# Performance work log

Measured on AMD Instinct MI355X. Metric: run time of the kernel, lower is better.

## Reference

```python
import jax, jax.numpy as jnp
import numpy as np

MASK_FILL = -99999.0  # value used by masked_fill_ in the torch source


def setup_inputs() -> dict:
    key = jax.random.key(0)
    k1, k2, k3, k4, k5, k6, k7 = jax.random.split(key, 7)
    B, S, H = 8, 2048, 1024
    query = jax.random.normal(k1, (B, S, H), dtype=jnp.float32)
    key_t = jax.random.normal(k2, (B, S, H), dtype=jnp.float32)
    value = jax.random.normal(k3, (B, S, H), dtype=jnp.float32)
    mask = jax.random.randint(k4, (B, S), 0, 2, dtype=jnp.int32)
    s = 1.0 / np.sqrt(H)
    Wq = jax.random.uniform(k5, (H, H), dtype=jnp.float32, minval=-s, maxval=s)
    Wk = jax.random.uniform(k6, (H, H), dtype=jnp.float32, minval=-s, maxval=s)
    Wv = jax.random.uniform(k7, (H, H), dtype=jnp.float32, minval=-s, maxval=s)
    return {"query": query, "key": key_t, "value": value,
            "Wq": Wq, "Wk": Wk, "Wv": Wv, "mask": mask}


def reference(query, key, value, Wq, Wk, Wv, mask):
    # Linear(h,h,bias=False): y = x @ W.T
    q = jnp.einsum('bsh,oh->bso', query, Wq)
    k = jnp.einsum('bsh,oh->bso', key, Wk)
    v = jnp.einsum('bsh,oh->bso', value, Wv)
    # score[b,i,j] = q[b,i,:] . k[b,j,:]  (NO 1/sqrt(d) scaling in source)
    score = jnp.einsum('bqh,bkh->bqk', q, k)
    # mask: [B, S_k] -> [B, 1, S_k]; positions where mask==0 get MASK_FILL
    m = mask[:, None, :]
    score = jnp.where(m == 0, jnp.float32(MASK_FILL), score)
    attn = jax.nn.softmax(score, axis=-1)
    context = jnp.einsum('bqk,bkh->bqh', attn, v)
    return context
```

## Files before the change

### kernel.cpp

```cpp
#include <hip/hip_runtime.h>
#include <hip/hip_fp16.h>
#include <math.h>

typedef _Float16 f16;
typedef _Float16 f16x4 __attribute__((ext_vector_type(4)));
typedef _Float16 f16x8 __attribute__((ext_vector_type(8)));
typedef float f32x4 __attribute__((ext_vector_type(4)));

#define GLOAD_LDS16(g, l)                                                                  \
    __builtin_amdgcn_global_load_lds((const __attribute__((address_space(1))) void*)(g),   \
                                     (__attribute__((address_space(3))) void*)(l), 16, 0, 0)

__global__ __launch_bounds__(256) void cast3_kernel(const float* __restrict__ s0,
                                                    const float* __restrict__ s1,
                                                    const float* __restrict__ s2,
                                                    f16* d0, f16* d1, f16* d2, int n16each)
{
    const int z = blockIdx.z;
    const float* src = (z == 0) ? s0 : (z == 1) ? s1 : s2;
    f16* dst = (z == 0) ? d0 : (z == 1) ? d1 : d2;
    const int stride = gridDim.x * blockDim.x;
    for (int i = blockIdx.x * blockDim.x + threadIdx.x; i < n16each; i += stride) {
        const float4* sp = (const float4*)(src + (long long)i * 16);
        float4 a = sp[0], b = sp[1], c = sp[2], d4 = sp[3];
        f16x8 lo = {(f16)a.x, (f16)a.y, (f16)a.z, (f16)a.w,
                    (f16)b.x, (f16)b.y, (f16)b.z, (f16)b.w};
        f16x8 hi = {(f16)c.x, (f16)c.y, (f16)c.z, (f16)c.w,
                    (f16)d4.x, (f16)d4.y, (f16)d4.z, (f16)d4.w};
        f16x8* dp = (f16x8*)(dst + (long long)i * 16);
        dp[0] = lo;
        dp[1] = hi;
    }
}

template <int OUTF16, int TRANSC>
__global__ __launch_bounds__(512, 2) void gemm_nt_k(
    const f16* __restrict__ Ab, const f16* __restrict__ Bb, void* __restrict__ Cb,
    int K, int lda, int ldb, int ldc,
    long long sA, long long sB, long long sC, int gx)
{
    __shared__ __align__(16) f16 smem[256 * 64 + 128 * 64];

    const int nwg = gridDim.x;
    const int swz = (blockIdx.x & 7) * (nwg >> 3) + (blockIdx.x >> 3);
    const int bx = swz % gx, by = swz / gx;

    const int z = blockIdx.z;
    const char* pA = (const char*)(Ab + z * sA + (long long)by * 256 * lda);
    const char* pB = (const char*)(Bb + z * sB + (long long)bx * 128 * ldb);
    const long long lda2 = (long long)lda * 2, ldb2 = (long long)ldb * 2;

    const int tid = threadIdx.x;
    const int w = tid >> 6, l = tid & 63;
    const int wr = w >> 1, wc = w & 1;

    f32x4 acc[4][4];
#pragma unroll
    for (int i = 0; i < 4; i++)
#pragma unroll
        for (int j = 0; j < 4; j++) acc[i][j] = (f32x4){0.f, 0.f, 0.f, 0.f};

    const int lr = l & 15;
    const int lkb = (l >> 4) * 16;

#define FRAG_A(row, kbyte)                                                                \
    (*(const f16x8*)((const char*)&smem[0] + ((row) * 128) + ((kbyte) ^ (((row) & 7) << 4))))
#define FRAG_B(row, kbyte)                                                                \
    (*(const f16x8*)((const char*)&smem[0] + 32768 + ((row) * 128) + ((kbyte) ^ (((row) & 7) << 4))))

    const int nt = K >> 6;
    for (int t = 0; t < nt; ++t) {
        const long long kb = (long long)t * 128;
#pragma unroll
        for (int i = 0; i < 4; i++) {
            const int c = i * 512 + tid;
            const int row = c >> 3;
            const int col = ((c & 7) * 16) ^ ((row & 7) << 4);
            GLOAD_LDS16(pA + (long long)row * lda2 + kb + col, &smem[(long long)c * 8]);
        }
#pragma unroll
        for (int i = 0; i < 2; i++) {
            const int c = i * 512 + tid;
            const int row = c >> 3;
            const int col = ((c & 7) * 16) ^ ((row & 7) << 4);
            GLOAD_LDS16(pB + (long long)row * ldb2 + kb + col, &smem[16384 + (long long)c * 8]);
        }
        __syncthreads();

        f16x8 bf[4][2], af[4][2];
#pragma unroll
        for (int fc = 0; fc < 4; fc++)
#pragma unroll
            for (int ks = 0; ks < 2; ks++)
                bf[fc][ks] = FRAG_B(wc * 64 + fc * 16 + lr, ks * 64 + lkb);
#pragma unroll
        for (int fq = 0; fq < 4; fq++)
#pragma unroll
            for (int ks = 0; ks < 2; ks++)
                af[fq][ks] = FRAG_A(wr * 64 + fq * 16 + lr, ks * 64 + lkb);

#pragma unroll
        for (int fq = 0; fq < 4; fq++)
#pragma unroll
            for (int fc = 0; fc < 4; fc++)
#pragma unroll
                for (int ks = 0; ks < 2; ks++)
                    acc[fq][fc] = __builtin_amdgcn_mfma_f32_16x16x32_f16(
                        af[fq][ks], bf[fc][ks], acc[fq][fc], 0, 0, 0);

        __syncthreads();
    }
#undef FRAG_A
#undef FRAG_B

    const int row_l = (l >> 4) * 4;
    const long long gr0 = (long long)by * 256 + wr * 64;
    const int gc0 = bx * 128 + wc * 64;

    if (TRANSC) {
        const long long blk_r0 = (long long)by * 256;
        const int b = (int)(blk_r0 >> 11);
        const int s_base = (int)(blk_r0 & 2047);
        f16* vTp = (f16*)Cb + (long long)b * 1024 * 2048;
#pragma unroll
        for (int h = 0; h < 2; h++) {
            __syncthreads();
            if ((wr >> 1) == h) {
                const int s64 = (wr & 1) * 64;
#pragma unroll
                for (int fq = 0; fq < 4; fq++)
#pragma unroll
                    for (int fc = 0; fc < 4; fc++)
#pragma unroll
                        for (int i = 0; i < 4; i++)
                            smem[(wc * 64 + fc * 16 + lr) * 136 + s64 + fq * 16 + row_l + i] =
                                (f16)acc[fq][fc][i];
            }
            __syncthreads();
#pragma unroll
            for (int j = 0; j < 4; j++) {
                const int c = j * 512 + tid;
                const int o = c >> 4, s8 = (c & 15) * 8;
                f16x8 vv = *(const f16x8*)&smem[o * 136 + s8];
                *(f16x8*)&vTp[((long long)(bx * 128 + o)) * 2048 + s_base + h * 128 + s8] = vv;
            }
        }
    } else if (OUTF16) {
        f16* C = (f16*)Cb + z * sC;
#pragma unroll
        for (int fq = 0; fq < 4; fq++)
#pragma unroll
            for (int fc = 0; fc < 4; fc++)
#pragma unroll
                for (int i = 0; i < 4; i++)
                    C[(gr0 + fq * 16 + row_l + i) * ldc + gc0 + fc * 16 + lr] = (f16)acc[fq][fc][i];
    } else {
        float* C = (float*)Cb + z * sC;
#pragma unroll
        for (int fq = 0; fq < 4; fq++)
#pragma unroll
            for (int fc = 0; fc < 4; fc++)
#pragma unroll
                for (int i = 0; i < 4; i++)
                    C[(gr0 + fq * 16 + row_l + i) * ldc + gc0 + fc * 16 + lr] = acc[fq][fc][i];
    }
}

__device__ __forceinline__ float wred_max(float v) {
#pragma unroll
    for (int o = 32; o > 0; o >>= 1) v = fmaxf(v, __shfl_xor(v, o));
    return v;
}
__device__ __forceinline__ float wred_sum(float v) {
#pragma unroll
    for (int o = 32; o > 0; o >>= 1) v += __shfl_xor(v, o);
    return v;
}

__global__ __launch_bounds__(256) void softmax_kernel(f16* __restrict__ Sm, const int* __restrict__ mask)
{
    const long long row = blockIdx.x;
    const int b = (int)(row >> 11);
    f16* Srow = Sm + row * 2048;
    const int* mrow = mask + b * 2048;
    const int t = threadIdx.x;
    const int w = t >> 6, l = t & 63;

    f16x8 sv = *(const f16x8*)(Srow + t * 8);
    int4 m0 = *(const int4*)(mrow + t * 8);
    int4 m1 = *(const int4*)(mrow + t * 8 + 4);
    int mk[8] = {m0.x, m0.y, m0.z, m0.w, m1.x, m1.y, m1.z, m1.w};
    float v[8];
#pragma unroll
    for (int j = 0; j < 8; j++) v[j] = (float)sv[j];

    float mx = -INFINITY;
#pragma unroll
    for (int j = 0; j < 8; j++) if (mk[j]) mx = fmaxf(mx, v[j]);
    mx = wred_max(mx);
    __shared__ float redm[4], reds[4];
    if (l == 0) redm[w] = mx;
    __syncthreads();
    mx = fmaxf(fmaxf(redm[0], redm[1]), fmaxf(redm[2], redm[3]));

    if (mx == -INFINITY) {
        const f16 u = (f16)(1.0f / 2048.0f);
        f16x8 pv;
#pragma unroll
        for (int j = 0; j < 8; j++) pv[j] = u;
        *(f16x8*)(Srow + t * 8) = pv;
        return;
    }

    float e[8];
    float s = 0.f;
#pragma unroll
    for (int j = 0; j < 8; j++) { e[j] = mk[j] ? expf(v[j] - mx) : 0.f; s += e[j]; }
    s = wred_sum(s);
    if (l == 0) reds[w] = s;
    __syncthreads();
    s = reds[0] + reds[1] + reds[2] + reds[3];
    const float inv = 1.0f / s;
    f16x8 pv;
#pragma unroll
    for (int j = 0; j < 8; j++) pv[j] = (f16)(e[j] * inv);
    *(f16x8*)(Srow + t * 8) = pv;
}

extern "C" void kernel_launch(void* const* d_in, const int* in_sizes, int n_in,
                              void* d_out, int out_size, void* d_ws, size_t ws_size,
                              hipStream_t stream)
{
    const float* query = (const float*)d_in[0];
    const float* keyi  = (const float*)d_in[1];
    const float* value = (const float*)d_in[2];
    const float* Wq    = (const float*)d_in[3];
    const float* Wk    = (const float*)d_in[4];
    const float* Wv    = (const float*)d_in[5];
    const int*   mask  = (const int*)d_in[6];
    float* out = (float*)d_out;

    const long long SH = (long long)8 * 2048 * 1024;
    f16* slot0 = (f16*)d_ws;
    f16* slot1 = slot0 + SH;
    f16* slot2 = slot0 + 2 * SH;
    f16* slot3 = slot0 + 3 * SH;
    f16* slot4 = slot0 + 4 * SH;
    f16* wh    = slot1;
    f16* Pb    = slot0;

    const int n16x = (int)(SH / 16);
    const int n16w = 1024 * 1024 / 16;
    const long long zero = 0;
    const long long M1 = 1024 * 1024;

    cast3_kernel<<<dim3(64, 1, 3), 256, 0, stream>>>(Wq, Wk, Wv, wh, wh + M1, wh + 2 * M1, n16w);
    cast3_kernel<<<dim3(1024, 1, 3), 256, 0, stream>>>(query, keyi, value, slot3, slot0, slot2, n16x);
    gemm_nt_k<1, 1><<<dim3(512, 1, 1), 512, 0, stream>>>(
        slot2, wh + 2 * M1, (void*)slot4, 1024, 1024, 1024, 2048, zero, zero, zero, 8);
    gemm_nt_k<1, 0><<<dim3(512, 1, 1), 512, 0, stream>>>(
        slot3, wh, (void*)slot2, 1024, 1024, 1024, 1024, zero, zero, zero, 8);
    gemm_nt_k<1, 0><<<dim3(512, 1, 1), 512, 0, stream>>>(
        slot0, wh + M1, (void*)slot3, 1024, 1024, 1024, 1024, zero, zero, zero, 8);
    gemm_nt_k<1, 0><<<dim3(128, 1, 8), 512, 0, stream>>>(
        slot2, slot3, (void*)Pb, 1024, 1024, 1024, 2048,
        (long long)2048 * 1024, (long long)2048 * 1024, (long long)2048 * 2048, 16);
    softmax_kernel<<<dim3(16384), 256, 0, stream>>>(Pb, mask);
    gemm_nt_k<0, 0><<<dim3(64, 1, 8), 512, 0, stream>>>(
        Pb, slot4, (void*)out, 2048, 2048, 2048, 1024,
        (long long)2048 * 2048, (long long)1024 * 2048, (long long)2048 * 1024, 8);
}
```

Before: 325.2 us.

## Fuse fp32-to-fp16 activation cast into projection GEMM A-tile loads

Removes the separate cast pass over query/key/value. The projection GEMMs now load fp32 A tiles straight into LDS with a wider swizzle and convert to fp16 when building fragments. This saves writing and re-reading three fp16 activation copies. In exchange it doubles the A tile's LDS footprint to 64KB plus 16KB for B, which may lower occupancy below two blocks per CU, and it adds conversion ALU work in the inner loop.

Measured after the change: 623.0 us. 91.6% more time.

```diff
diff --git a/kernel.cpp b/kernel.cpp
--- a/kernel.cpp
+++ b/kernel.cpp
@@ -33,22 +33,25 @@
     }
 }
 
-template <int OUTF16, int TRANSC>
+template <int OUTF16, int TRANSC, int AF32>
 __global__ __launch_bounds__(512, 2) void gemm_nt_k(
-    const f16* __restrict__ Ab, const f16* __restrict__ Bb, void* __restrict__ Cb,
+    const void* __restrict__ Ab, const f16* __restrict__ Bb, void* __restrict__ Cb,
     int K, int lda, int ldb, int ldc,
     long long sA, long long sB, long long sC, int gx)
 {
-    __shared__ __align__(16) f16 smem[256 * 64 + 128 * 64];
+    __shared__ __align__(16) f16 smem[AF32 ? (256 * 128 + 128 * 64) : (256 * 64 + 128 * 64)];
+    constexpr int B_OFF_E = AF32 ? 256 * 128 : 256 * 64;
+    constexpr int B_OFF_B = B_OFF_E * 2;
 
     const int nwg = gridDim.x;
     const int swz = (blockIdx.x & 7) * (nwg >> 3) + (blockIdx.x >> 3);
     const int bx = swz % gx, by = swz / gx;
 
     const int z = blockIdx.z;
-    const char* pA = (const char*)(Ab + z * sA + (long long)by * 256 * lda);
+    constexpr int esz = AF32 ? 4 : 2;
+    const char* pA = (const char*)Ab + ((long long)z * sA + (long long)by * 256 * lda) * esz;
     const char* pB = (const char*)(Bb + z * sB + (long long)bx * 128 * ldb);
-    const long long lda2 = (long long)lda * 2, ldb2 = (long long)ldb * 2;
+    const long long ldaB = (long long)lda * esz, ldb2 = (long long)ldb * 2;
 
     const int tid = threadIdx.x;
     const int w = tid >> 6, l = tid & 63;
@@ -63,27 +66,40 @@
     const int lr = l & 15;
     const int lkb = (l >> 4) * 16;
 
-#define FRAG_A(row, kbyte)                                                                \
+#define FRAG_A16(row, kbyte)                                                              \
     (*(const f16x8*)((const char*)&smem[0] + ((row) * 128) + ((kbyte) ^ (((row) & 7) << 4))))
 #define FRAG_B(row, kbyte)                                                                \
-    (*(const f16x8*)((const char*)&smem[0] + 32768 + ((row) * 128) + ((kbyte) ^ (((row) & 7) << 4))))
+    (*(const f16x8*)((const char*)&smem[0] + B_OFF_B + ((row) * 128) + ((kbyte) ^ (((row) & 7) << 4))))
 
     const int nt = K >> 6;
     for (int t = 0; t < nt; ++t) {
-        const long long kb = (long long)t * 128;
-#pragma unroll
-        for (int i = 0; i < 4; i++) {
-            const int c = i * 512 + tid;
-            const int row = c >> 3;
-            const int col = ((c & 7) * 16) ^ ((row & 7) << 4);
-            GLOAD_LDS16(pA + (long long)row * lda2 + kb + col, &smem[(long long)c * 8]);
+        const long long kb = (long long)t * 64 * esz;
+        if (AF32) {
+#pragma unroll
+            for (int i = 0; i < 8; i++) {
+                const int c = i * 512 + tid;
+                const int row = c >> 4;
+                const int col = ((c & 15) * 16) ^ ((row & 7) << 5);
+                GLOAD_LDS16(pA + (long long)row * ldaB + kb + col, &smem[(long long)c * 8]);
+            }
+        } else {
+#pragma unroll
+            for (int i = 0; i < 4; i++) {
+                const int c = i * 512 + tid;
+                const int row = c >> 3;
+                const int col = ((c & 7) * 16) ^ ((row & 7) << 4);
+                GLOAD_LDS16(pA + (long long)row * ldaB + kb + col, &smem[(long long)c * 8]);
+            }
         }
-#pragma unroll
-        for (int i = 0; i < 2; i++) {
-            const int c = i * 512 + tid;
-            const int row = c >> 3;
-            const int col = ((c & 7) * 16) ^ ((row & 7) << 4);
-            GLOAD_LDS16(pB + (long long)row * ldb2 + kb + col, &smem[16384 + (long long)c * 8]);
+        {
+            const long long kbB = (long long)t * 128;
+#pragma unroll
+            for (int i = 0; i < 2; i++) {
+                const int c = i * 512 + tid;
+                const int row = c >> 3;
+                const int col = ((c & 7) * 16) ^ ((row & 7) << 4);
+                GLOAD_LDS16(pB + (long long)row * ldb2 + kbB + col, &smem[B_OFF_E + (long long)c * 8]);
+            }
         }
         __syncthreads();
 
@@ -96,8 +112,19 @@
 #pragma unroll
         for (int fq = 0; fq < 4; fq++)
 #pragma unroll
-            for (int ks = 0; ks < 2; ks++)
-                af[fq][ks] = FRAG_A(wr * 64 + fq * 16 + lr, ks * 64 + lkb);
+            for (int ks = 0; ks < 2; ks++) {
+                const int row = wr * 64 + fq * 16 + lr;
+                if (AF32) {
+                    const int g0 = 2 * (ks * 64 + lkb);
+                    const char* base = (const char*)&smem[0] + row * 256 + ((g0) ^ ((row & 7) << 5));
+                    float4 lo = *(const float4*)(base);
+                    float4 hi = *(const float4*)(base + 16);
+                    af[fq][ks] = (f16x8){(f16)lo.x, (f16)lo.y, (f16)lo.z, (f16)lo.w,
+                                         (f16)hi.x, (f16)hi.y, (f16)hi.z, (f16)hi.w};
+                } else {
+                    af[fq][ks] = FRAG_A16(row, ks * 64 + lkb);
+                }
+            }
 
 #pragma unroll
         for (int fq = 0; fq < 4; fq++)
@@ -110,7 +137,7 @@
 
         __syncthreads();
     }
-#undef FRAG_A
+#undef FRAG_A16
 #undef FRAG_B
 
     const int row_l = (l >> 4) * 4;
@@ -249,24 +276,22 @@
     f16* wh    = slot1;
     f16* Pb    = slot0;
 
-    const int n16x = (int)(SH / 16);
     const int n16w = 1024 * 1024 / 16;
     const long long zero = 0;
     const long long M1 = 1024 * 1024;
 
     cast3_kernel<<<dim3(64, 1, 3), 256, 0, stream>>>(Wq, Wk, Wv, wh, wh + M1, wh + 2 * M1, n16w);
-    cast3_kernel<<<dim3(1024, 1, 3), 256, 0, stream>>>(query, keyi, value, slot3, slot0, slot2, n16x);
-    gemm_nt_k<1, 1><<<dim3(512, 1, 1), 512, 0, stream>>>(
-        slot2, wh + 2 * M1, (void*)slot4, 1024, 1024, 1024, 2048, zero, zero, zero, 8);
-    gemm_nt_k<1, 0><<<dim3(512, 1, 1), 512, 0, stream>>>(
-        slot3, wh, (void*)slot2, 1024, 1024, 1024, 1024, zero, zero, zero, 8);
-    gemm_nt_k<1, 0><<<dim3(512, 1, 1), 512, 0, stream>>>(
-        slot0, wh + M1, (void*)slot3, 1024, 1024, 1024, 1024, zero, zero, zero, 8);
-    gemm_nt_k<1, 0><<<dim3(128, 1, 8), 512, 0, stream>>>(
-        slot2, slot3, (void*)Pb, 1024, 1024, 1024, 2048,
+    gemm_nt_k<1, 1, 1><<<dim3(512, 1, 1), 512, 0, stream>>>(
+        (const void*)value, wh + 2 * M1, (void*)slot4, 1024, 1024, 1024, 2048, zero, zero, zero, 8);
+    gemm_nt_k<1, 0, 1><<<dim3(512, 1, 1), 512, 0, stream>>>(
+        (const void*)query, wh, (void*)slot2, 1024, 1024, 1024, 1024, zero, zero, zero, 8);
+    gemm_nt_k<1, 0, 1><<<dim3(512, 1, 1), 512, 0, stream>>>(
+        (const void*)keyi, wh + M1, (void*)slot3, 1024, 1024, 1024, 1024, zero, zero, zero, 8);
+    gemm_nt_k<1, 0, 0><<<dim3(128, 1, 8), 512, 0, stream>>>(
+        (const void*)slot2, slot3, (void*)Pb, 1024, 1024, 1024, 2048,
         (long long)2048 * 1024, (long long)2048 * 1024, (long long)2048 * 2048, 16);
     softmax_kernel<<<dim3(16384), 256, 0, stream>>>(Pb, mask);
-    gemm_nt_k<0, 0><<<dim3(64, 1, 8), 512, 0, stream>>>(
-        Pb, slot4, (void*)out, 2048, 2048, 2048, 1024,
+    gemm_nt_k<0, 0, 0><<<dim3(64, 1, 8), 512, 0, stream>>>(
+        (const void*)Pb, slot4, (void*)out, 2048, 2048, 2048, 1024,
         (long long)2048 * 2048, (long long)1024 * 2048, (long long)2048 * 1024, 8);
 }
```

## Fold Wq and Wk into one product matrix to skip a projection GEMM

Applied to the files above, without the earlier changes.

Precomputes M = Wq^T Wk (as a 1024x1024 fp16 matrix) using a transpose-cast kernel and a small GEMM. The score matrix is then formed as query · (key M^T)^T, so only the key is projected and the raw fp16 query is used directly, removing one of the large 16384x1024x1024 projection GEMMs. In exchange it adds a small weight GEMM and a transpose pass, and the fp16 rounding of the combined matrix changes numerical error. Scores here have large magnitude with no scaling, which can make this more sensitive.

Result: no change. 323.9 us (-0.4%).

```diff
diff --git a/kernel.cpp b/kernel.cpp
--- a/kernel.cpp
+++ b/kernel.cpp
@@ -33,6 +33,35 @@
     }
 }
 
+__global__ __launch_bounds__(256) void transcast_w_kernel(const float* __restrict__ Wq,
+                                                          const float* __restrict__ Wk,
+                                                          f16* __restrict__ dA,
+                                                          f16* __restrict__ dB)
+{
+    __shared__ f16 tile[64][72];
+    const float* src = blockIdx.z ? Wk : Wq;
+    f16* dst = blockIdx.z ? dB : dA;
+    const int h0 = blockIdx.x * 64, o0 = blockIdx.y * 64;
+    const int t = threadIdx.x;
+    const int r = t >> 2, c = (t & 3) * 16;
+    const float* sp = src + (long long)(o0 + r) * 1024 + h0 + c;
+    float4 v0 = *(const float4*)(sp + 0);
+    float4 v1 = *(const float4*)(sp + 4);
+    float4 v2 = *(const float4*)(sp + 8);
+    float4 v3 = *(const float4*)(sp + 12);
+    *(f16x4*)&tile[r][c]      = (f16x4){(f16)v0.x, (f16)v0.y, (f16)v0.z, (f16)v0.w};
+    *(f16x4*)&tile[r][c + 4]  = (f16x4){(f16)v1.x, (f16)v1.y, (f16)v1.z, (f16)v1.w};
+    *(f16x4*)&tile[r][c + 8]  = (f16x4){(f16)v2.x, (f16)v2.y, (f16)v2.z, (f16)v2.w};
+    *(f16x4*)&tile[r][c + 12] = (f16x4){(f16)v3.x, (f16)v3.y, (f16)v3.z, (f16)v3.w};
+    __syncthreads();
+    f16 buf[16];
+#pragma unroll
+    for (int j = 0; j < 16; j++) buf[j] = tile[c + j][r];
+    f16* dp = dst + (long long)(h0 + r) * 1024 + o0 + c;
+    *(f16x8*)(dp)     = *(f16x8*)&buf[0];
+    *(f16x8*)(dp + 8) = *(f16x8*)&buf[8];
+}
+
 template <int OUTF16, int TRANSC>
 __global__ __launch_bounds__(512, 2) void gemm_nt_k(
     const f16* __restrict__ Ab, const f16* __restrict__ Bb, void* __restrict__ Cb,
@@ -40,6 +69,8 @@
     long long sA, long long sB, long long sC, int gx)
 {
     __shared__ __align__(16) f16 smem[256 * 64 + 128 * 64];
+    constexpr int B_OFF_E = 256 * 64;
+    constexpr int B_OFF_B = B_OFF_E * 2;
 
     const int nwg = gridDim.x;
     const int swz = (blockIdx.x & 7) * (nwg >> 3) + (blockIdx.x >> 3);
@@ -63,10 +94,10 @@
     const int lr = l & 15;
     const int lkb = (l >> 4) * 16;
 
-#define FRAG_A(row, kbyte)                                                                \
+#define FRAG_A16(row, kbyte)                                                              \
     (*(const f16x8*)((const char*)&smem[0] + ((row) * 128) + ((kbyte) ^ (((row) & 7) << 4))))
 #define FRAG_B(row, kbyte)                                                                \
-    (*(const f16x8*)((const char*)&smem[0] + 32768 + ((row) * 128) + ((kbyte) ^ (((row) & 7) << 4))))
+    (*(const f16x8*)((const char*)&smem[0] + B_OFF_B + ((row) * 128) + ((kbyte) ^ (((row) & 7) << 4))))
 
     const int nt = K >> 6;
     for (int t = 0; t < nt; ++t) {
@@ -83,7 +114,7 @@
             const int c = i * 512 + tid;
             const int row = c >> 3;
             const int col = ((c & 7) * 16) ^ ((row & 7) << 4);
-            GLOAD_LDS16(pB + (long long)row * ldb2 + kb + col, &smem[16384 + (long long)c * 8]);
+            GLOAD_LDS16(pB + (long long)row * ldb2 + kb + col, &smem[B_OFF_E + (long long)c * 8]);
         }
         __syncthreads();
 
@@ -97,7 +128,7 @@
         for (int fq = 0; fq < 4; fq++)
 #pragma unroll
             for (int ks = 0; ks < 2; ks++)
-                af[fq][ks] = FRAG_A(wr * 64 + fq * 16 + lr, ks * 64 + lkb);
+                af[fq][ks] = FRAG_A16(wr * 64 + fq * 16 + lr, ks * 64 + lkb);
 
 #pragma unroll
         for (int fq = 0; fq < 4; fq++)
@@ -110,7 +141,7 @@
 
         __syncthreads();
     }
-#undef FRAG_A
+#undef FRAG_A16
 #undef FRAG_B
 
     const int row_l = (l >> 4) * 4;
@@ -246,22 +277,26 @@
     f16* slot2 = slot0 + 2 * SH;
     f16* slot3 = slot0 + 3 * SH;
     f16* slot4 = slot0 + 4 * SH;
-    f16* wh    = slot1;
-    f16* Pb    = slot0;
+    const long long M1 = 1024 * 1024;
+    f16* whA = slot1;
+    f16* whB = slot1 + M1;
+    f16* whC = slot1 + 2 * M1;
+    f16* whD = slot1 + 3 * M1;
+    f16* Pb  = slot0;
 
     const int n16x = (int)(SH / 16);
-    const int n16w = 1024 * 1024 / 16;
+    const int n16w = (int)(M1 / 16);
     const long long zero = 0;
-    const long long M1 = 1024 * 1024;
-
-    cast3_kernel<<<dim3(64, 1, 3), 256, 0, stream>>>(Wq, Wk, Wv, wh, wh + M1, wh + 2 * M1, n16w);
-    cast3_kernel<<<dim3(1024, 1, 3), 256, 0, stream>>>(query, keyi, value, slot3, slot0, slot2, n16x);
+
+    transcast_w_kernel<<<dim3(16, 16, 2), 256, 0, stream>>>(Wq, Wk, whA, whB);
+    cast3_kernel<<<dim3(64, 1, 1), 256, 0, stream>>>(Wv, Wv, Wv, whC, whC, whC, n16w);
+    gemm_nt_k<1, 0><<<dim3(32, 1, 1), 512, 0, stream>>>(
+        whA, whB, (void*)whD, 1024, 1024, 1024, 1024, zero, zero, zero, 8);
+    cast3_kernel<<<dim3(1024, 1, 3), 256, 0, stream>>>(query, keyi, value, slot2, slot0, slot3, n16x);
     gemm_nt_k<1, 1><<<dim3(512, 1, 1), 512, 0, stream>>>(
-        slot2, wh + 2 * M1, (void*)slot4, 1024, 1024, 1024, 2048, zero, zero, zero, 8);
+        slot3, whC, (void*)slot4, 1024, 1024, 1024, 2048, zero, zero, zero, 8);
     gemm_nt_k<1, 0><<<dim3(512, 1, 1), 512, 0, stream>>>(
-        slot3, wh, (void*)slot2, 1024, 1024, 1024, 1024, zero, zero, zero, 8);
-    gemm_nt_k<1, 0><<<dim3(512, 1, 1), 512, 0, stream>>>(
-        slot0, wh + M1, (void*)slot3, 1024, 1024, 1024, 1024, zero, zero, zero, 8);
+        slot0, whD, (void*)slot3, 1024, 1024, 1024, 1024, zero, zero, zero, 8);
     gemm_nt_k<1, 0><<<dim3(128, 1, 8), 512, 0, stream>>>(
         slot2, slot3, (void*)Pb, 1024, 1024, 1024, 2048,
         (long long)2048 * 1024, (long long)2048 * 1024, (long long)2048 * 2048, 16);
```
